# Optimization experiments

Hardware: AMD Instinct MI355X
Metric: run time of the kernel (lower is better)

## Reference

```python
import jax, jax.numpy as jnp
import numpy as np

DIM = 128        # channel dim C
N = 784          # H*W = 28*28 = max_seq_len
PBD = 128        # position_bias_dim
FF = 4 * DIM
EPS_LN = 1e-5


def layer_norm(x, g, b):
    mu = jnp.mean(x, axis=-1, keepdims=True)
    var = jnp.mean((x - mu) ** 2, axis=-1, keepdims=True)
    return (x - mu) * jax.lax.rsqrt(var + EPS_LN) * g + b


def setup_inputs() -> dict:
    key = jax.random.key(0)
    ks = jax.random.split(key, 12)
    s = 0.02
    return {
        "x": jax.random.normal(ks[0], (1, DIM, 28, 28), dtype=jnp.float32),
        "wq": jax.random.normal(ks[1], (DIM, DIM), dtype=jnp.float32) * s,
        "wk": jax.random.normal(ks[2], (DIM, DIM), dtype=jnp.float32) * s,
        "wv": jax.random.normal(ks[3], (DIM, DIM), dtype=jnp.float32) * s,
        "wo": jax.random.normal(ks[4], (DIM, DIM), dtype=jnp.float32) * s,
        "bo": jnp.zeros((DIM,), dtype=jnp.float32),
        "u": jax.random.normal(ks[5], (N, PBD), dtype=jnp.float32) * 0.01,
        "v": jax.random.normal(ks[6], (N, PBD), dtype=jnp.float32) * 0.01,
        "ln1_g": jnp.ones((DIM,), dtype=jnp.float32),
        "ln1_b": jnp.zeros((DIM,), dtype=jnp.float32),
        "ln2_g": jnp.ones((DIM,), dtype=jnp.float32),
        "ln2_b": jnp.zeros((DIM,), dtype=jnp.float32),
        "w1": jax.random.normal(ks[7], (FF, DIM), dtype=jnp.float32) * s,
        "b1": jnp.zeros((FF,), dtype=jnp.float32),
        "w2": jax.random.normal(ks[8], (DIM, FF), dtype=jnp.float32) * s,
        "b2": jnp.zeros((DIM,), dtype=jnp.float32),
    }


def reference(x, wq, wk, wv, wo, bo, u, v, ln1_g, ln1_b, ln2_g, ln2_b, w1, b1, w2, b2):
    B, C, H, W = x.shape
    t = x.reshape(B, C, H * W).transpose(0, 2, 1)  # [B, N, C]

    # --- AFT-Full attention block ---
    xn = layer_norm(t, ln1_g, ln1_b)
    q = jax.nn.sigmoid(xn @ wq.T)                  # [B, N, D]
    k = xn @ wk.T                                  # [B, N, D]
    vv = xn @ wv.T                                 # [B, N, D]
    pos_bias = u @ v.T                             # [N, N] (query n, key m)
    logits = k[:, None, :, :] + pos_bias[None, :, :, None]  # [B, N, M, D]
    attn = jax.nn.softmax(logits, axis=2)          # softmax over key axis m
    ctx = jnp.einsum('bnmd,bmd->bnd', attn, vv)    # weighted sum over keys
    out = q * ctx                                  # sigmoid gate (dropout=identity)
    out = out @ wo.T + bo
    t = t + out

    # --- MLP block ---
    fn = layer_norm(t, ln2_g, ln2_b)
    ff = jax.nn.gelu(fn @ w1.T + b1, approximate=False) @ w2.T + b2
    t = t + ff

    return t.transpose(0, 2, 1).reshape(B, C, H, W)
```

## Files before the change

kernel.cpp:

```cpp
#include <hip/hip_runtime.h>
#include <math.h>

#define NTOK 784
#define DIM 128
#define FFD 512

__global__ __launch_bounds__(256) void posw_qkv3(
    const float* __restrict__ pu, const float* __restrict__ pv, float* __restrict__ W,
    const float* __restrict__ x, const float* __restrict__ g, const float* __restrict__ b,
    const float* __restrict__ wq, const float* __restrict__ wk, const float* __restrict__ wv,
    float* __restrict__ q, float* __restrict__ ek, float* __restrict__ vv) {
  __shared__ float smem[12288];
  int tid = threadIdx.x;

  if (blockIdx.x < 325) {
    float (*As)[32] = (float(*)[32])smem;
    float (*Bs)[64] = (float(*)[64])(smem + 4096);
    int m0 = (blockIdx.x % 25) * 32, n0 = (blockIdx.x / 25) * 64;
    {
      int r = tid >> 3, kq = (tid & 7) * 16;
      int gm = min(m0 + r, NTOK - 1);
#pragma unroll
      for (int j = 0; j < 4; ++j) {
        float4 a = *(const float4*)&pu[gm * DIM + kq + j * 4];
        As[kq + j * 4 + 0][r] = a.x; As[kq + j * 4 + 1][r] = a.y;
        As[kq + j * 4 + 2][r] = a.z; As[kq + j * 4 + 3][r] = a.w;
      }
      int rb = tid >> 2, kb = (tid & 3) * 32;
      int gn = min(n0 + rb, NTOK - 1);
#pragma unroll
      for (int j = 0; j < 8; ++j) {
        float4 v = *(const float4*)&pv[gn * DIM + kb + j * 4];
        Bs[kb + j * 4 + 0][rb] = v.x; Bs[kb + j * 4 + 1][rb] = v.y;
        Bs[kb + j * 4 + 2][rb] = v.z; Bs[kb + j * 4 + 3][rb] = v.w;
      }
    }
    __syncthreads();
    int tx = tid & 15, ty = tid >> 4;
    float acc[2][4] = {};
#pragma unroll 8
    for (int kk = 0; kk < DIM; ++kk) {
      float2 a2 = *(const float2*)&As[kk][ty * 2];
      float4 b4 = *(const float4*)&Bs[kk][tx * 4];
      float av[2] = {a2.x, a2.y};
      float bv[4] = {b4.x, b4.y, b4.z, b4.w};
#pragma unroll
      for (int i = 0; i < 2; ++i)
#pragma unroll
        for (int j = 0; j < 4; ++j) acc[i][j] = fmaf(av[i], bv[j], acc[i][j]);
    }
    int c0 = n0 + tx * 4;
    if (c0 + 3 < NTOK) {
#pragma unroll
      for (int i = 0; i < 2; ++i) {
        int gr = m0 + ty * 2 + i;
        if (gr < NTOK) {
          float4 o = {expf(acc[i][0]), expf(acc[i][1]), expf(acc[i][2]), expf(acc[i][3])};
          *(float4*)&W[gr * NTOK + c0] = o;
        }
      }
    }
  } else {
    float (*Xs)[32] = (float(*)[32])smem;
    float (*Bq)[64] = (float(*)[64])(smem + 4096);
    float* redS = smem + 8192;
    float* redQ = smem + 8448;
    int bid = blockIdx.x - 325;
    int m0 = (bid % 25) * 32;
    int ct = bid / 25;
    int wsel = ct >> 1;
    int n0 = (ct & 1) * 64;
    const float* B = (wsel == 0) ? wq : (wsel == 1) ? wk : wv;

    if (m0 + 32 <= NTOK) {
#pragma unroll
      for (int it = 0; it < 4; ++it) {
        int idx = it * 256 + tid;
        int c = idx >> 3, j4 = (idx & 7) * 4;
        float4 v = *(const float4*)&x[c * NTOK + m0 + j4];
        Xs[c][j4 + 0] = v.x; Xs[c][j4 + 1] = v.y; Xs[c][j4 + 2] = v.z; Xs[c][j4 + 3] = v.w;
      }
    } else {
#pragma unroll
      for (int it = 0; it < 4; ++it) {
        int idx = it * 256 + tid;
        int c = idx >> 3, j4 = (idx & 7) * 4;
#pragma unroll
        for (int u = 0; u < 4; ++u) {
          int n = min(m0 + j4 + u, NTOK - 1);
          Xs[c][j4 + u] = x[c * NTOK + n];
        }
      }
    }
    __syncthreads();

    int n = tid & 31, grp = tid >> 5;
    float s = 0.f, ss = 0.f;
    for (int c = grp * 16; c < grp * 16 + 16; ++c) { float v = Xs[c][n]; s += v; ss += v * v; }
    redS[grp * 32 + n] = s; redQ[grp * 32 + n] = ss;
    __syncthreads();
    float sum = 0.f, sq = 0.f;
#pragma unroll
    for (int gi = 0; gi < 8; ++gi) { sum += redS[gi * 32 + n]; sq += redQ[gi * 32 + n]; }
    float mu = sum * (1.0f / DIM);
    float var = sq * (1.0f / DIM) - mu * mu;
    float rs = rsqrtf(var + 1e-5f);
    for (int c = grp * 16; c < grp * 16 + 16; ++c)
      Xs[c][n] = (Xs[c][n] - mu) * rs * g[c] + b[c];

    int tx = tid & 15, ty = tid >> 4;
    float acc[2][4] = {};
#pragma unroll
    for (int h = 0; h < 2; ++h) {
      {
        int r = tid >> 2, kq = (tid & 3) * 16;
#pragma unroll
        for (int j = 0; j < 4; ++j) {
          float4 v = *(const float4*)&B[(n0 + r) * DIM + h * 64 + kq + j * 4];
          Bq[kq + j * 4 + 0][r] = v.x; Bq[kq + j * 4 + 1][r] = v.y;
          Bq[kq + j * 4 + 2][r] = v.z; Bq[kq + j * 4 + 3][r] = v.w;
        }
      }
      __syncthreads();
#pragma unroll 4
      for (int kk = 0; kk < 64; ++kk) {
        float2 a2 = *(const float2*)&Xs[h * 64 + kk][ty * 2];
        float4 b4 = *(const float4*)&Bq[kk][tx * 4];
        float av[2] = {a2.x, a2.y};
        float bv[4] = {b4.x, b4.y, b4.z, b4.w};
#pragma unroll
        for (int i = 0; i < 2; ++i)
#pragma unroll
          for (int j = 0; j < 4; ++j) acc[i][j] = fmaf(av[i], bv[j], acc[i][j]);
      }
      __syncthreads();
    }
    int c0 = n0 + tx * 4;
    float* dst = (wsel == 0) ? q : (wsel == 1) ? ek : vv;
#pragma unroll
    for (int i = 0; i < 2; ++i) {
      int gr = m0 + ty * 2 + i;
      if (gr < NTOK) {
        float4 o;
        if (wsel == 0) {
          o.x = 1.0f / (1.0f + expf(-acc[i][0]));
          o.y = 1.0f / (1.0f + expf(-acc[i][1]));
          o.z = 1.0f / (1.0f + expf(-acc[i][2]));
          o.w = 1.0f / (1.0f + expf(-acc[i][3]));
        } else if (wsel == 1) {
          o.x = expf(acc[i][0]); o.y = expf(acc[i][1]);
          o.z = expf(acc[i][2]); o.w = expf(acc[i][3]);
        } else {
          o.x = acc[i][0]; o.y = acc[i][1]; o.z = acc[i][2]; o.w = acc[i][3];
        }
        *(float4*)&dst[gr * DIM + c0] = o;
      }
    }
  }
}

__global__ __launch_bounds__(256) void agg32(
    const float* __restrict__ W, const float* __restrict__ ek,
    const float* __restrict__ vv, float* __restrict__ nump, float* __restrict__ denp) {
  __shared__ float As[96][32];
  __shared__ float Bn[96][64];
  __shared__ float Bd[96][64];
  int tid = threadIdx.x;
  int m0 = blockIdx.x * 32, d0 = blockIdx.y * 64, sp = blockIdx.z;
  int tx = tid & 15, ty = tid >> 4;
  int ra = tid >> 3, ka = (tid & 7) * 4;
  int kb = tid >> 3, db = (tid & 7) * 8;
  int gm = min(m0 + ra, NTOK - 1);
  float an[2][4] = {}, ad[2][4] = {};
  int tlo = (sp * 25) / 8, thi = ((sp + 1) * 25) / 8;
  for (int base = tlo; base < thi; base += 3) {
    int nt = min(3, thi - base);
    for (int t = 0; t < nt; ++t) {
      int k0 = (base + t) * 32;
      int lk = t * 32;
      if (k0 + 32 <= NTOK) {
        float4 a = *(const float4*)&W[gm * NTOK + k0 + ka];
        As[lk + ka + 0][ra] = a.x; As[lk + ka + 1][ra] = a.y;
        As[lk + ka + 2][ra] = a.z; As[lk + ka + 3][ra] = a.w;
        int gk = k0 + kb;
        float4 e0 = *(const float4*)&ek[gk * DIM + d0 + db];
        float4 e1 = *(const float4*)&ek[gk * DIM + d0 + db + 4];
        float4 w0 = *(const float4*)&vv[gk * DIM + d0 + db];
        float4 w1_ = *(const float4*)&vv[gk * DIM + d0 + db + 4];
        Bd[lk + kb][db + 0] = e0.x; Bd[lk + kb][db + 1] = e0.y;
        Bd[lk + kb][db + 2] = e0.z; Bd[lk + kb][db + 3] = e0.w;
        Bd[lk + kb][db + 4] = e1.x; Bd[lk + kb][db + 5] = e1.y;
        Bd[lk + kb][db + 6] = e1.z; Bd[lk + kb][db + 7] = e1.w;
        Bn[lk + kb][db + 0] = e0.x * w0.x; Bn[lk + kb][db + 1] = e0.y * w0.y;
        Bn[lk + kb][db + 2] = e0.z * w0.z; Bn[lk + kb][db + 3] = e0.w * w0.w;
        Bn[lk + kb][db + 4] = e1.x * w1_.x; Bn[lk + kb][db + 5] = e1.y * w1_.y;
        Bn[lk + kb][db + 6] = e1.z * w1_.z; Bn[lk + kb][db + 7] = e1.w * w1_.w;
      } else {
#pragma unroll
        for (int j = 0; j < 4; ++j) {
          int gk = k0 + ka + j;
          As[lk + ka + j][ra] = (gk < NTOK) ? W[gm * NTOK + gk] : 0.f;
        }
        int gk = k0 + kb;
        if (gk < NTOK) {
          float4 e0 = *(const float4*)&ek[gk * DIM + d0 + db];
          float4 e1 = *(const float4*)&ek[gk * DIM + d0 + db + 4];
          float4 w0 = *(const float4*)&vv[gk * DIM + d0 + db];
          float4 w1_ = *(const float4*)&vv[gk * DIM + d0 + db + 4];
          Bd[lk + kb][db + 0] = e0.x; Bd[lk + kb][db + 1] = e0.y;
          Bd[lk + kb][db + 2] = e0.z; Bd[lk + kb][db + 3] = e0.w;
          Bd[lk + kb][db + 4] = e1.x; Bd[lk + kb][db + 5] = e1.y;
          Bd[lk + kb][db + 6] = e1.z; Bd[lk + kb][db + 7] = e1.w;
          Bn[lk + kb][db + 0] = e0.x * w0.x; Bn[lk + kb][db + 1] = e0.y * w0.y;
          Bn[lk + kb][db + 2] = e0.z * w0.z; Bn[lk + kb][db + 3] = e0.w * w0.w;
          Bn[lk + kb][db + 4] = e1.x * w1_.x; Bn[lk + kb][db + 5] = e1.y * w1_.y;
          Bn[lk + kb][db + 6] = e1.z * w1_.z; Bn[lk + kb][db + 7] = e1.w * w1_.w;
        } else {
#pragma unroll
          for (int j = 0; j < 8; ++j) { Bd[lk + kb][db + j] = 0.f; Bn[lk + kb][db + j] = 0.f; }
        }
      }
    }
    __syncthreads();
    int nk = nt * 32;
    for (int kk = 0; kk < nk; ++kk) {
      float2 a2 = *(const float2*)&As[kk][ty * 2];
      float4 n4 = *(const float4*)&Bn[kk][tx * 4];
      float4 d4 = *(const float4*)&Bd[kk][tx * 4];
      float av[2] = {a2.x, a2.y};
      float nv[4] = {n4.x, n4.y, n4.z, n4.w};
      float dv[4] = {d4.x, d4.y, d4.z, d4.w};
#pragma unroll
      for (int i = 0; i < 2; ++i)
#pragma unroll
        for (int j = 0; j < 4; ++j) {
          an[i][j] = fmaf(av[i], nv[j], an[i][j]);
          ad[i][j] = fmaf(av[i], dv[j], ad[i][j]);
        }
    }
    __syncthreads();
  }
#pragma unroll
  for (int i = 0; i < 2; ++i) {
    int gr = m0 + ty * 2 + i;
    if (gr < NTOK) {
      float4 on = {an[i][0], an[i][1], an[i][2], an[i][3]};
      float4 od = {ad[i][0], ad[i][1], ad[i][2], ad[i][3]};
      *(float4*)&nump[(sp * NTOK + gr) * DIM + d0 + tx * 4] = on;
      *(float4*)&denp[(sp * NTOK + gr) * DIM + d0 + tx * 4] = od;
    }
  }
}

__global__ __launch_bounds__(256) void gate_proj_ln(
    const float* __restrict__ q, const float* __restrict__ nump,
    const float* __restrict__ denp, const float* __restrict__ wo,
    const float* __restrict__ bo, const float* __restrict__ x,
    const float* __restrict__ g2, const float* __restrict__ b2n,
    const float* __restrict__ b2f, float* __restrict__ fn, float* __restrict__ out) {
  __shared__ float At[DIM][9];
  __shared__ float Bs[DIM][DIM];
  int tid = threadIdx.x;
  int m0 = blockIdx.x * 8;

  {
    int nn = tid >> 5, c4 = (tid & 31) * 4;
    int base = (m0 + nn) * DIM + c4;
    float4 qv = *(const float4*)&q[base];
    float4 nv = {0.f, 0.f, 0.f, 0.f}, dv = {0.f, 0.f, 0.f, 0.f};
#pragma unroll
    for (int s = 0; s < 8; ++s) {
      float4 a = *(const float4*)&nump[s * NTOK * DIM + base];
      float4 d = *(const float4*)&denp[s * NTOK * DIM + base];
      nv.x += a.x; nv.y += a.y; nv.z += a.z; nv.w += a.w;
      dv.x += d.x; dv.y += d.y; dv.z += d.z; dv.w += d.w;
    }
    At[c4 + 0][nn] = qv.x * (nv.x / dv.x);
    At[c4 + 1][nn] = qv.y * (nv.y / dv.y);
    At[c4 + 2][nn] = qv.z * (nv.z / dv.z);
    At[c4 + 3][nn] = qv.w * (nv.w / dv.w);
  }
  {
    int r = tid >> 1, kq = (tid & 1) * 64;
#pragma unroll
    for (int j = 0; j < 16; ++j) {
      float4 v = *(const float4*)&wo[r * DIM + kq + j * 4];
      Bs[kq + j * 4 + 0][r] = v.x; Bs[kq + j * 4 + 1][r] = v.y;
      Bs[kq + j * 4 + 2][r] = v.z; Bs[kq + j * 4 + 3][r] = v.w;
    }
  }
  __syncthreads();

  int ty = tid >> 5, tx = tid & 31;
  float acc[4] = {0.f, 0.f, 0.f, 0.f};
#pragma unroll 4
  for (int kk = 0; kk < DIM; ++kk) {
    float a = At[kk][ty];
    float4 b4 = *(const float4*)&Bs[kk][tx * 4];
    acc[0] = fmaf(a, b4.x, acc[0]);
    acc[1] = fmaf(a, b4.y, acc[1]);
    acc[2] = fmaf(a, b4.z, acc[2]);
    acc[3] = fmaf(a, b4.w, acc[3]);
  }
  int gn = m0 + ty;
  int c0 = tx * 4;
  float4 bias = *(const float4*)&bo[c0];
  float o0 = acc[0] + bias.x + x[(c0 + 0) * NTOK + gn];
  float o1 = acc[1] + bias.y + x[(c0 + 1) * NTOK + gn];
  float o2 = acc[2] + bias.z + x[(c0 + 2) * NTOK + gn];
  float o3 = acc[3] + bias.w + x[(c0 + 3) * NTOK + gn];

  float4 bf = *(const float4*)&b2f[c0];
  out[(c0 + 0) * NTOK + gn] = o0 + bf.x;
  out[(c0 + 1) * NTOK + gn] = o1 + bf.y;
  out[(c0 + 2) * NTOK + gn] = o2 + bf.z;
  out[(c0 + 3) * NTOK + gn] = o3 + bf.w;

  float s = o0 + o1 + o2 + o3;
  float ss = o0 * o0 + o1 * o1 + o2 * o2 + o3 * o3;
#pragma unroll
  for (int off = 1; off < 32; off <<= 1) {
    s += __shfl_xor(s, off);
    ss += __shfl_xor(ss, off);
  }
  float mu = s * (1.0f / DIM);
  float var = ss * (1.0f / DIM) - mu * mu;
  float rs = rsqrtf(var + 1e-5f);
  float4 gg = *(const float4*)&g2[c0];
  float4 bb = *(const float4*)&b2n[c0];
  float4 f;
  f.x = (o0 - mu) * rs * gg.x + bb.x;
  f.y = (o1 - mu) * rs * gg.y + bb.y;
  f.z = (o2 - mu) * rs * gg.z + bb.z;
  f.w = (o3 - mu) * rs * gg.w + bb.w;
  *(float4*)&fn[gn * DIM + c0] = f;
}

__global__ __launch_bounds__(256) void ff_fused16(
    const float* __restrict__ fn, const float* __restrict__ w1,
    const float* __restrict__ b1f, const float* __restrict__ w2,
    float* __restrict__ out) {
  __shared__ float Fs[DIM][16];
  __shared__ float W1s[DIM][64];
  __shared__ float P[16][65];
  int tid = threadIdx.x;
  int m0 = blockIdx.x * 16, f0 = blockIdx.y * 64;

  {
    int r = tid >> 4, kq = (tid & 15) * 8;
#pragma unroll
    for (int j = 0; j < 2; ++j) {
      float4 v = *(const float4*)&fn[(m0 + r) * DIM + kq + j * 4];
      Fs[kq + j * 4 + 0][r] = v.x; Fs[kq + j * 4 + 1][r] = v.y;
      Fs[kq + j * 4 + 2][r] = v.z; Fs[kq + j * 4 + 3][r] = v.w;
    }
    int rw = tid >> 2, kw = (tid & 3) * 32;
#pragma unroll
    for (int j = 0; j < 8; ++j) {
      float4 v = *(const float4*)&w1[(f0 + rw) * DIM + kw + j * 4];
      W1s[kw + j * 4 + 0][rw] = v.x; W1s[kw + j * 4 + 1][rw] = v.y;
      W1s[kw + j * 4 + 2][rw] = v.z; W1s[kw + j * 4 + 3][rw] = v.w;
    }
  }
  __syncthreads();

  int row = tid >> 4, f4 = (tid & 15) * 4;
  float acc1[4] = {};
#pragma unroll 4
  for (int kk = 0; kk < DIM; ++kk) {
    float a = Fs[kk][row];
    float4 b4 = *(const float4*)&W1s[kk][f4];
    acc1[0] = fmaf(a, b4.x, acc1[0]);
    acc1[1] = fmaf(a, b4.y, acc1[1]);
    acc1[2] = fmaf(a, b4.z, acc1[2]);
    acc1[3] = fmaf(a, b4.w, acc1[3]);
  }
  float4 b1v = *(const float4*)&b1f[f0 + f4];
  float bb[4] = {b1v.x, b1v.y, b1v.z, b1v.w};
  float ge[4];
#pragma unroll
  for (int j = 0; j < 4; ++j) {
    float v = acc1[j] + bb[j];
    ge[j] = 0.5f * v * (1.0f + erff(v * 0.70710678118654752f));
  }
  __syncthreads();

#pragma unroll
  for (int j = 0; j < 4; ++j) P[row][f4 + j] = ge[j];
  float* W2s = &W1s[0][0];
  {
    int c = tid >> 1, fq = (tid & 1) * 32;
#pragma unroll
    for (int j = 0; j < 8; ++j) {
      float4 v = *(const float4*)&w2[c * FFD + f0 + fq + j * 4];
      W2s[(fq + j * 4 + 0) * DIM + c] = v.x;
      W2s[(fq + j * 4 + 1) * DIM + c] = v.y;
      W2s[(fq + j * 4 + 2) * DIM + c] = v.z;
      W2s[(fq + j * 4 + 3) * DIM + c] = v.w;
    }
  }
  __syncthreads();

  int r2 = tid & 15, cb = (tid >> 4) * 8;
  float acc2[8] = {};
  for (int f = 0; f < 64; ++f) {
    float pvv = P[r2][f];
    const float* wr = &W2s[f * DIM + cb];
#pragma unroll
    for (int j4 = 0; j4 < 2; ++j4) {
      float4 wv = *(const float4*)&wr[j4 * 4];
      acc2[j4 * 4 + 0] = fmaf(pvv, wv.x, acc2[j4 * 4 + 0]);
      acc2[j4 * 4 + 1] = fmaf(pvv, wv.y, acc2[j4 * 4 + 1]);
      acc2[j4 * 4 + 2] = fmaf(pvv, wv.z, acc2[j4 * 4 + 2]);
      acc2[j4 * 4 + 3] = fmaf(pvv, wv.w, acc2[j4 * 4 + 3]);
    }
  }
#pragma unroll
  for (int j = 0; j < 8; ++j)
    atomicAdd(&out[(cb + j) * NTOK + m0 + r2], acc2[j]);
}

extern "C" void kernel_launch(void* const* d_in, const int* in_sizes, int n_in,
                              void* d_out, int out_size, void* d_ws, size_t ws_size,
                              hipStream_t stream) {
  const float* x   = (const float*)d_in[0];
  const float* wq  = (const float*)d_in[1];
  const float* wk  = (const float*)d_in[2];
  const float* wv  = (const float*)d_in[3];
  const float* wo  = (const float*)d_in[4];
  const float* bo  = (const float*)d_in[5];
  const float* pu  = (const float*)d_in[6];
  const float* pv  = (const float*)d_in[7];
  const float* g1  = (const float*)d_in[8];
  const float* b1n = (const float*)d_in[9];
  const float* g2  = (const float*)d_in[10];
  const float* b2n = (const float*)d_in[11];
  const float* w1  = (const float*)d_in[12];
  const float* b1f = (const float*)d_in[13];
  const float* w2  = (const float*)d_in[14];
  const float* b2f = (const float*)d_in[15];
  float* out = (float*)d_out;

  float* ws = (float*)d_ws;
  float* q    = ws;
  float* ek   = ws + 100352;
  float* vv   = ws + 200704;
  float* fn   = ws + 301056;
  float* W    = ws + 401408;
  float* nump = ws + 1016064;
  float* denp = ws + 1818880;

  posw_qkv3<<<475, 256, 0, stream>>>(pu, pv, W, x, g1, b1n, wq, wk, wv, q, ek, vv);
  agg32<<<dim3(25, 2, 8), 256, 0, stream>>>(W, ek, vv, nump, denp);
  gate_proj_ln<<<98, 256, 0, stream>>>(q, nump, denp, wo, bo, x, g2, b2n, b2f, fn, out);
  ff_fused16<<<dim3(49, 8), 256, 0, stream>>>(fn, w1, b1f, w2, out);
}
```

Before: 50.35 us.

## Fuse gate/out-projection/LN2 with the MLP into one kernel and zero output early

Merges the gate+output projection+LayerNorm kernel with the fused MLP kernel, so each of the 8 FF-slice blocks per 8-token tile recomputes the attention gate, the Wo projection and LN2 in shared memory instead of writing and re-reading the normalized activations. The output buffer is zeroed inside the first kernel, and the residual is folded into the blockIdx.y==0 atomic contribution. This removes one kernel launch and the fn round trip through global memory. In exchange the Wo projection and the nump/denp reduction are repeated eight times, shared memory grows to about 70KB, and the FF tiles shrink to 8 tokens, which may lower occupancy.

```diff
diff --git a/kernel.cpp b/kernel.cpp
--- a/kernel.cpp
+++ b/kernel.cpp
@@ -9,9 +9,12 @@
     const float* __restrict__ pu, const float* __restrict__ pv, float* __restrict__ W,
     const float* __restrict__ x, const float* __restrict__ g, const float* __restrict__ b,
     const float* __restrict__ wq, const float* __restrict__ wk, const float* __restrict__ wv,
-    float* __restrict__ q, float* __restrict__ ek, float* __restrict__ vv) {
+    float* __restrict__ q, float* __restrict__ ek, float* __restrict__ vv,
+    float* __restrict__ out) {
   __shared__ float smem[12288];
   int tid = threadIdx.x;
+
+  for (int i = blockIdx.x * 256 + tid; i < NTOK * DIM; i += 475 * 256) out[i] = 0.f;
 
   if (blockIdx.x < 325) {
     float (*As)[32] = (float(*)[32])smem;
@@ -252,16 +255,21 @@
   }
 }
 
-__global__ __launch_bounds__(256) void gate_proj_ln(
+__global__ __launch_bounds__(256) void epi_fused(
     const float* __restrict__ q, const float* __restrict__ nump,
     const float* __restrict__ denp, const float* __restrict__ wo,
     const float* __restrict__ bo, const float* __restrict__ x,
     const float* __restrict__ g2, const float* __restrict__ b2n,
-    const float* __restrict__ b2f, float* __restrict__ fn, float* __restrict__ out) {
+    const float* __restrict__ w1, const float* __restrict__ b1f,
+    const float* __restrict__ w2, const float* __restrict__ b2f,
+    float* __restrict__ out) {
   __shared__ float At[DIM][9];
-  __shared__ float Bs[DIM][DIM];
+  __shared__ float Ws[DIM * DIM];
+  __shared__ float Fn[DIM][9];
+  __shared__ float P[64][9];
   int tid = threadIdx.x;
   int m0 = blockIdx.x * 8;
+  int f0 = blockIdx.y * 64;
 
   {
     int nn = tid >> 5, c4 = (tid & 31) * 4;
@@ -285,139 +293,109 @@
 #pragma unroll
     for (int j = 0; j < 16; ++j) {
       float4 v = *(const float4*)&wo[r * DIM + kq + j * 4];
-      Bs[kq + j * 4 + 0][r] = v.x; Bs[kq + j * 4 + 1][r] = v.y;
-      Bs[kq + j * 4 + 2][r] = v.z; Bs[kq + j * 4 + 3][r] = v.w;
+      Ws[(kq + j * 4 + 0) * DIM + r] = v.x; Ws[(kq + j * 4 + 1) * DIM + r] = v.y;
+      Ws[(kq + j * 4 + 2) * DIM + r] = v.z; Ws[(kq + j * 4 + 3) * DIM + r] = v.w;
     }
   }
   __syncthreads();
 
-  int ty = tid >> 5, tx = tid & 31;
-  float acc[4] = {0.f, 0.f, 0.f, 0.f};
+  int row = tid >> 5, c4 = (tid & 31) * 4;
+  int gn = m0 + row;
+  float tv[4];
+  {
+    float acc[4] = {0.f, 0.f, 0.f, 0.f};
 #pragma unroll 4
-  for (int kk = 0; kk < DIM; ++kk) {
-    float a = At[kk][ty];
-    float4 b4 = *(const float4*)&Bs[kk][tx * 4];
-    acc[0] = fmaf(a, b4.x, acc[0]);
-    acc[1] = fmaf(a, b4.y, acc[1]);
-    acc[2] = fmaf(a, b4.z, acc[2]);
-    acc[3] = fmaf(a, b4.w, acc[3]);
-  }
-  int gn = m0 + ty;
-  int c0 = tx * 4;
-  float4 bias = *(const float4*)&bo[c0];
-  float o0 = acc[0] + bias.x + x[(c0 + 0) * NTOK + gn];
-  float o1 = acc[1] + bias.y + x[(c0 + 1) * NTOK + gn];
-  float o2 = acc[2] + bias.z + x[(c0 + 2) * NTOK + gn];
-  float o3 = acc[3] + bias.w + x[(c0 + 3) * NTOK + gn];
-
-  float4 bf = *(const float4*)&b2f[c0];
-  out[(c0 + 0) * NTOK + gn] = o0 + bf.x;
-  out[(c0 + 1) * NTOK + gn] = o1 + bf.y;
-  out[(c0 + 2) * NTOK + gn] = o2 + bf.z;
-  out[(c0 + 3) * NTOK + gn] = o3 + bf.w;
-
-  float s = o0 + o1 + o2 + o3;
-  float ss = o0 * o0 + o1 * o1 + o2 * o2 + o3 * o3;
-#pragma unroll
-  for (int off = 1; off < 32; off <<= 1) {
-    s += __shfl_xor(s, off);
-    ss += __shfl_xor(ss, off);
-  }
-  float mu = s * (1.0f / DIM);
-  float var = ss * (1.0f / DIM) - mu * mu;
-  float rs = rsqrtf(var + 1e-5f);
-  float4 gg = *(const float4*)&g2[c0];
-  float4 bb = *(const float4*)&b2n[c0];
-  float4 f;
-  f.x = (o0 - mu) * rs * gg.x + bb.x;
-  f.y = (o1 - mu) * rs * gg.y + bb.y;
-  f.z = (o2 - mu) * rs * gg.z + bb.z;
-  f.w = (o3 - mu) * rs * gg.w + bb.w;
-  *(float4*)&fn[gn * DIM + c0] = f;
-}
-
-__global__ __launch_bounds__(256) void ff_fused16(
-    const float* __restrict__ fn, const float* __restrict__ w1,
-    const float* __restrict__ b1f, const float* __restrict__ w2,
-    float* __restrict__ out) {
-  __shared__ float Fs[DIM][16];
-  __shared__ float W1s[DIM][64];
-  __shared__ float P[16][65];
-  int tid = threadIdx.x;
-  int m0 = blockIdx.x * 16, f0 = blockIdx.y * 64;
-
-  {
-    int r = tid >> 4, kq = (tid & 15) * 8;
-#pragma unroll
-    for (int j = 0; j < 2; ++j) {
-      float4 v = *(const float4*)&fn[(m0 + r) * DIM + kq + j * 4];
-      Fs[kq + j * 4 + 0][r] = v.x; Fs[kq + j * 4 + 1][r] = v.y;
-      Fs[kq + j * 4 + 2][r] = v.z; Fs[kq + j * 4 + 3][r] = v.w;
-    }
+    for (int kk = 0; kk < DIM; ++kk) {
+      float a = At[kk][row];
+      float4 b4 = *(const float4*)&Ws[kk * DIM + c4];
+      acc[0] = fmaf(a, b4.x, acc[0]);
+      acc[1] = fmaf(a, b4.y, acc[1]);
+      acc[2] = fmaf(a, b4.z, acc[2]);
+      acc[3] = fmaf(a, b4.w, acc[3]);
+    }
+    float4 bias = *(const float4*)&bo[c4];
+    float o0 = acc[0] + bias.x + x[(c4 + 0) * NTOK + gn];
+    float o1 = acc[1] + bias.y + x[(c4 + 1) * NTOK + gn];
+    float o2 = acc[2] + bias.z + x[(c4 + 2) * NTOK + gn];
+    float o3 = acc[3] + bias.w + x[(c4 + 3) * NTOK + gn];
+    float4 bf = *(const float4*)&b2f[c4];
+    tv[0] = o0 + bf.x; tv[1] = o1 + bf.y; tv[2] = o2 + bf.z; tv[3] = o3 + bf.w;
+
+    float s = o0 + o1 + o2 + o3;
+    float ss = o0 * o0 + o1 * o1 + o2 * o2 + o3 * o3;
+#pragma unroll
+    for (int off = 1; off < 32; off <<= 1) {
+      s += __shfl_xor(s, off);
+      ss += __shfl_xor(ss, off);
+    }
+    float mu = s * (1.0f / DIM);
+    float var = ss * (1.0f / DIM) - mu * mu;
+    float rs = rsqrtf(var + 1e-5f);
+    float4 gg = *(const float4*)&g2[c4];
+    float4 bb = *(const float4*)&b2n[c4];
+    Fn[c4 + 0][row] = (o0 - mu) * rs * gg.x + bb.x;
+    Fn[c4 + 1][row] = (o1 - mu) * rs * gg.y + bb.y;
+    Fn[c4 + 2][row] = (o2 - mu) * rs * gg.z + bb.z;
+    Fn[c4 + 3][row] = (o3 - mu) * rs * gg.w + bb.w;
+  }
+  __syncthreads();
+
+  {
     int rw = tid >> 2, kw = (tid & 3) * 32;
 #pragma unroll
     for (int j = 0; j < 8; ++j) {
       float4 v = *(const float4*)&w1[(f0 + rw) * DIM + kw + j * 4];
-      W1s[kw + j * 4 + 0][rw] = v.x; W1s[kw + j * 4 + 1][rw] = v.y;
-      W1s[kw + j * 4 + 2][rw] = v.z; W1s[kw + j * 4 + 3][rw] = v.w;
-    }
-  }
-  __syncthreads();
-
-  int row = tid >> 4, f4 = (tid & 15) * 4;
-  float acc1[4] = {};
-#pragma unroll 4
-  for (int kk = 0; kk < DIM; ++kk) {
-    float a = Fs[kk][row];
-    float4 b4 = *(const float4*)&W1s[kk][f4];
-    acc1[0] = fmaf(a, b4.x, acc1[0]);
-    acc1[1] = fmaf(a, b4.y, acc1[1]);
-    acc1[2] = fmaf(a, b4.z, acc1[2]);
-    acc1[3] = fmaf(a, b4.w, acc1[3]);
-  }
-  float4 b1v = *(const float4*)&b1f[f0 + f4];
-  float bb[4] = {b1v.x, b1v.y, b1v.z, b1v.w};
-  float ge[4];
-#pragma unroll
-  for (int j = 0; j < 4; ++j) {
-    float v = acc1[j] + bb[j];
-    ge[j] = 0.5f * v * (1.0f + erff(v * 0.70710678118654752f));
-  }
-  __syncthreads();
-
-#pragma unroll
-  for (int j = 0; j < 4; ++j) P[row][f4 + j] = ge[j];
-  float* W2s = &W1s[0][0];
-  {
+      Ws[(kw + j * 4 + 0) * 64 + rw] = v.x; Ws[(kw + j * 4 + 1) * 64 + rw] = v.y;
+      Ws[(kw + j * 4 + 2) * 64 + rw] = v.z; Ws[(kw + j * 4 + 3) * 64 + rw] = v.w;
+    }
+    float* W2s = Ws + 8192;
     int c = tid >> 1, fq = (tid & 1) * 32;
 #pragma unroll
     for (int j = 0; j < 8; ++j) {
       float4 v = *(const float4*)&w2[c * FFD + f0 + fq + j * 4];
-      W2s[(fq + j * 4 + 0) * DIM + c] = v.x;
-      W2s[(fq + j * 4 + 1) * DIM + c] = v.y;
-      W2s[(fq + j * 4 + 2) * DIM + c] = v.z;
-      W2s[(fq + j * 4 + 3) * DIM + c] = v.w;
+      W2s[(fq + j * 4 + 0) * DIM + c] = v.x; W2s[(fq + j * 4 + 1) * DIM + c] = v.y;
+      W2s[(fq + j * 4 + 2) * DIM + c] = v.z; W2s[(fq + j * 4 + 3) * DIM + c] = v.w;
     }
   }
   __syncthreads();
 
-  int r2 = tid & 15, cb = (tid >> 4) * 8;
-  float acc2[8] = {};
-  for (int f = 0; f < 64; ++f) {
-    float pvv = P[r2][f];
-    const float* wr = &W2s[f * DIM + cb];
-#pragma unroll
-    for (int j4 = 0; j4 < 2; ++j4) {
-      float4 wv = *(const float4*)&wr[j4 * 4];
-      acc2[j4 * 4 + 0] = fmaf(pvv, wv.x, acc2[j4 * 4 + 0]);
-      acc2[j4 * 4 + 1] = fmaf(pvv, wv.y, acc2[j4 * 4 + 1]);
-      acc2[j4 * 4 + 2] = fmaf(pvv, wv.z, acc2[j4 * 4 + 2]);
-      acc2[j4 * 4 + 3] = fmaf(pvv, wv.w, acc2[j4 * 4 + 3]);
-    }
-  }
-#pragma unroll
-  for (int j = 0; j < 8; ++j)
-    atomicAdd(&out[(cb + j) * NTOK + m0 + r2], acc2[j]);
+  {
+    int f2 = (tid & 31) * 2;
+    float a0 = 0.f, a1 = 0.f;
+#pragma unroll 4
+    for (int kk = 0; kk < DIM; ++kk) {
+      float a = Fn[kk][row];
+      float2 w = *(const float2*)&Ws[kk * 64 + f2];
+      a0 = fmaf(a, w.x, a0);
+      a1 = fmaf(a, w.y, a1);
+    }
+    float2 b1v = *(const float2*)&b1f[f0 + f2];
+    float v0 = a0 + b1v.x, v1 = a1 + b1v.y;
+    P[f2 + 0][row] = 0.5f * v0 * (1.0f + erff(v0 * 0.70710678118654752f));
+    P[f2 + 1][row] = 0.5f * v1 * (1.0f + erff(v1 * 0.70710678118654752f));
+  }
+  __syncthreads();
+
+  {
+    const float* W2s = Ws + 8192;
+    float acc[4] = {0.f, 0.f, 0.f, 0.f};
+#pragma unroll 4
+    for (int f = 0; f < 64; ++f) {
+      float p = P[f][row];
+      float4 w4 = *(const float4*)&W2s[f * DIM + c4];
+      acc[0] = fmaf(p, w4.x, acc[0]);
+      acc[1] = fmaf(p, w4.y, acc[1]);
+      acc[2] = fmaf(p, w4.z, acc[2]);
+      acc[3] = fmaf(p, w4.w, acc[3]);
+    }
+    if (blockIdx.y == 0) {
+      acc[0] += tv[0]; acc[1] += tv[1]; acc[2] += tv[2]; acc[3] += tv[3];
+    }
+    atomicAdd(&out[(c4 + 0) * NTOK + gn], acc[0]);
+    atomicAdd(&out[(c4 + 1) * NTOK + gn], acc[1]);
+    atomicAdd(&out[(c4 + 2) * NTOK + gn], acc[2]);
+    atomicAdd(&out[(c4 + 3) * NTOK + gn], acc[3]);
+  }
 }
 
 extern "C" void kernel_launch(void* const* d_in, const int* in_sizes, int n_in,
@@ -445,13 +423,12 @@
   float* q    = ws;
   float* ek   = ws + 100352;
   float* vv   = ws + 200704;
-  float* fn   = ws + 301056;
-  float* W    = ws + 401408;
-  float* nump = ws + 1016064;
-  float* denp = ws + 1818880;
-
-  posw_qkv3<<<475, 256, 0, stream>>>(pu, pv, W, x, g1, b1n, wq, wk, wv, q, ek, vv);
+  float* W    = ws + 301056;
+  float* nump = ws + 915712;
+  float* denp = ws + 1718528;
+
+  posw_qkv3<<<475, 256, 0, stream>>>(pu, pv, W, x, g1, b1n, wq, wk, wv, q, ek, vv, out);
   agg32<<<dim3(25, 2, 8), 256, 0, stream>>>(W, ek, vv, nump, denp);
-  gate_proj_ln<<<98, 256, 0, stream>>>(q, nump, denp, wo, bo, x, g2, b2n, b2f, fn, out);
-  ff_fused16<<<dim3(49, 8), 256, 0, stream>>>(fn, w1, b1f, w2, out);
+  epi_fused<<<dim3(98, 8), 256, 0, stream>>>(q, nump, denp, wo, bo, x, g2, b2n,
+                                             w1, b1f, w2, b2f, out);
 }
```

Result: slower. 77.76 us (+54.4%).

## Replace split-K aggregation with full-K per-block reduction and fuse gating

Applied to the files above, without the earlier changes.

The aggregation kernel no longer splits the key dimension into 8 partial sums. Each block now holds 8 full rows of the positional-weight matrix in shared memory, iterates over all 784 keys with register prefetch of the next ek/vv tile, and applies the sigmoid gate and division in place, writing the final attention output. This removes the large partial-sum buffers and the reduction pass in the projection kernel. The cost is a smaller grid of 196 blocks with low per-thread arithmetic (2 columns each), about 33KB of shared memory per block, and a longer serial loop per block.

```diff
diff --git a/kernel.cpp b/kernel.cpp
--- a/kernel.cpp
+++ b/kernel.cpp
@@ -159,102 +159,97 @@
   }
 }
 
-__global__ __launch_bounds__(256) void agg32(
+__global__ __launch_bounds__(256) void agg_full(
     const float* __restrict__ W, const float* __restrict__ ek,
-    const float* __restrict__ vv, float* __restrict__ nump, float* __restrict__ denp) {
-  __shared__ float As[96][32];
-  __shared__ float Bn[96][64];
-  __shared__ float Bd[96][64];
+    const float* __restrict__ vv, const float* __restrict__ q,
+    float* __restrict__ attn) {
+  __shared__ float Wt[8 * 784];
+  __shared__ float Bd[32][68];
+  __shared__ float Bn[32][68];
   int tid = threadIdx.x;
-  int m0 = blockIdx.x * 32, d0 = blockIdx.y * 64, sp = blockIdx.z;
-  int tx = tid & 15, ty = tid >> 4;
-  int ra = tid >> 3, ka = (tid & 7) * 4;
-  int kb = tid >> 3, db = (tid & 7) * 8;
-  int gm = min(m0 + ra, NTOK - 1);
-  float an[2][4] = {}, ad[2][4] = {};
-  int tlo = (sp * 25) / 8, thi = ((sp + 1) * 25) / 8;
-  for (int base = tlo; base < thi; base += 3) {
-    int nt = min(3, thi - base);
-    for (int t = 0; t < nt; ++t) {
-      int k0 = (base + t) * 32;
-      int lk = t * 32;
-      if (k0 + 32 <= NTOK) {
-        float4 a = *(const float4*)&W[gm * NTOK + k0 + ka];
-        As[lk + ka + 0][ra] = a.x; As[lk + ka + 1][ra] = a.y;
-        As[lk + ka + 2][ra] = a.z; As[lk + ka + 3][ra] = a.w;
-        int gk = k0 + kb;
-        float4 e0 = *(const float4*)&ek[gk * DIM + d0 + db];
-        float4 e1 = *(const float4*)&ek[gk * DIM + d0 + db + 4];
-        float4 w0 = *(const float4*)&vv[gk * DIM + d0 + db];
-        float4 w1_ = *(const float4*)&vv[gk * DIM + d0 + db + 4];
-        Bd[lk + kb][db + 0] = e0.x; Bd[lk + kb][db + 1] = e0.y;
-        Bd[lk + kb][db + 2] = e0.z; Bd[lk + kb][db + 3] = e0.w;
-        Bd[lk + kb][db + 4] = e1.x; Bd[lk + kb][db + 5] = e1.y;
-        Bd[lk + kb][db + 6] = e1.z; Bd[lk + kb][db + 7] = e1.w;
-        Bn[lk + kb][db + 0] = e0.x * w0.x; Bn[lk + kb][db + 1] = e0.y * w0.y;
-        Bn[lk + kb][db + 2] = e0.z * w0.z; Bn[lk + kb][db + 3] = e0.w * w0.w;
-        Bn[lk + kb][db + 4] = e1.x * w1_.x; Bn[lk + kb][db + 5] = e1.y * w1_.y;
-        Bn[lk + kb][db + 6] = e1.z * w1_.z; Bn[lk + kb][db + 7] = e1.w * w1_.w;
-      } else {
-#pragma unroll
-        for (int j = 0; j < 4; ++j) {
-          int gk = k0 + ka + j;
-          As[lk + ka + j][ra] = (gk < NTOK) ? W[gm * NTOK + gk] : 0.f;
-        }
-        int gk = k0 + kb;
-        if (gk < NTOK) {
-          float4 e0 = *(const float4*)&ek[gk * DIM + d0 + db];
-          float4 e1 = *(const float4*)&ek[gk * DIM + d0 + db + 4];
-          float4 w0 = *(const float4*)&vv[gk * DIM + d0 + db];
-          float4 w1_ = *(const float4*)&vv[gk * DIM + d0 + db + 4];
-          Bd[lk + kb][db + 0] = e0.x; Bd[lk + kb][db + 1] = e0.y;
-          Bd[lk + kb][db + 2] = e0.z; Bd[lk + kb][db + 3] = e0.w;
-          Bd[lk + kb][db + 4] = e1.x; Bd[lk + kb][db + 5] = e1.y;
-          Bd[lk + kb][db + 6] = e1.z; Bd[lk + kb][db + 7] = e1.w;
-          Bn[lk + kb][db + 0] = e0.x * w0.x; Bn[lk + kb][db + 1] = e0.y * w0.y;
-          Bn[lk + kb][db + 2] = e0.z * w0.z; Bn[lk + kb][db + 3] = e0.w * w0.w;
-          Bn[lk + kb][db + 4] = e1.x * w1_.x; Bn[lk + kb][db + 5] = e1.y * w1_.y;
-          Bn[lk + kb][db + 6] = e1.z * w1_.z; Bn[lk + kb][db + 7] = e1.w * w1_.w;
-        } else {
-#pragma unroll
-          for (int j = 0; j < 8; ++j) { Bd[lk + kb][db + j] = 0.f; Bn[lk + kb][db + j] = 0.f; }
-        }
-      }
+  int m0 = blockIdx.x * 8, d0 = blockIdx.y * 64;
+
+#pragma unroll
+  for (int j = 0; j < 7; ++j) {
+    int idx = j * 256 + tid;
+    if (idx < 1568) {
+      int r = idx / 196, c4 = (idx % 196) * 4;
+      float4 a = *(const float4*)&W[(m0 + r) * NTOK + c4];
+      *(float4*)&Wt[r * 784 + c4] = a;
+    }
+  }
+
+  int ks = tid >> 4, d4 = (tid & 15) * 4;
+  float4 pe0, pe1, pv0, pv1;
+  {
+    pe0 = *(const float4*)&ek[(ks)*DIM + d0 + d4];
+    pv0 = *(const float4*)&vv[(ks)*DIM + d0 + d4];
+    pe1 = *(const float4*)&ek[(16 + ks) * DIM + d0 + d4];
+    pv1 = *(const float4*)&vv[(16 + ks) * DIM + d0 + d4];
+  }
+
+  int row = tid >> 5, c2 = (tid & 31) * 2;
+  float an0 = 0.f, an1 = 0.f, ad0 = 0.f, ad1 = 0.f;
+  const float* wr = &Wt[row * 784];
+
+  for (int c = 0; c < 25; ++c) {
+    int k0 = c * 32;
+    int nk = (k0 + 32 <= NTOK) ? 32 : (NTOK - k0);
+    if (ks < nk) {
+      Bd[ks][d4 + 0] = pe0.x; Bd[ks][d4 + 1] = pe0.y; Bd[ks][d4 + 2] = pe0.z; Bd[ks][d4 + 3] = pe0.w;
+      Bn[ks][d4 + 0] = pe0.x * pv0.x; Bn[ks][d4 + 1] = pe0.y * pv0.y;
+      Bn[ks][d4 + 2] = pe0.z * pv0.z; Bn[ks][d4 + 3] = pe0.w * pv0.w;
+    }
+    if (16 + ks < nk) {
+      Bd[16 + ks][d4 + 0] = pe1.x; Bd[16 + ks][d4 + 1] = pe1.y;
+      Bd[16 + ks][d4 + 2] = pe1.z; Bd[16 + ks][d4 + 3] = pe1.w;
+      Bn[16 + ks][d4 + 0] = pe1.x * pv1.x; Bn[16 + ks][d4 + 1] = pe1.y * pv1.y;
+      Bn[16 + ks][d4 + 2] = pe1.z * pv1.z; Bn[16 + ks][d4 + 3] = pe1.w * pv1.w;
     }
     __syncthreads();
-    int nk = nt * 32;
-    for (int kk = 0; kk < nk; ++kk) {
-      float2 a2 = *(const float2*)&As[kk][ty * 2];
-      float4 n4 = *(const float4*)&Bn[kk][tx * 4];
-      float4 d4 = *(const float4*)&Bd[kk][tx * 4];
-      float av[2] = {a2.x, a2.y};
-      float nv[4] = {n4.x, n4.y, n4.z, n4.w};
-      float dv[4] = {d4.x, d4.y, d4.z, d4.w};
-#pragma unroll
-      for (int i = 0; i < 2; ++i)
-#pragma unroll
-        for (int j = 0; j < 4; ++j) {
-          an[i][j] = fmaf(av[i], nv[j], an[i][j]);
-          ad[i][j] = fmaf(av[i], dv[j], ad[i][j]);
-        }
+    if (c < 24) {
+      int kn = (c + 1) * 32;
+      int nkn = (kn + 32 <= NTOK) ? 32 : (NTOK - kn);
+      if (ks < nkn) {
+        pe0 = *(const float4*)&ek[(kn + ks) * DIM + d0 + d4];
+        pv0 = *(const float4*)&vv[(kn + ks) * DIM + d0 + d4];
+      }
+      if (16 + ks < nkn) {
+        pe1 = *(const float4*)&ek[(kn + 16 + ks) * DIM + d0 + d4];
+        pv1 = *(const float4*)&vv[(kn + 16 + ks) * DIM + d0 + d4];
+      }
+    }
+    if (nk == 32) {
+#pragma unroll 8
+      for (int kk = 0; kk < 32; ++kk) {
+        float a = wr[k0 + kk];
+        float2 bn = *(const float2*)&Bn[kk][c2];
+        float2 bd = *(const float2*)&Bd[kk][c2];
+        an0 = fmaf(a, bn.x, an0); an1 = fmaf(a, bn.y, an1);
+        ad0 = fmaf(a, bd.x, ad0); ad1 = fmaf(a, bd.y, ad1);
+      }
+    } else {
+#pragma unroll 8
+      for (int kk = 0; kk < 16; ++kk) {
+        float a = wr[k0 + kk];
+        float2 bn = *(const float2*)&Bn[kk][c2];
+        float2 bd = *(const float2*)&Bd[kk][c2];
+        an0 = fmaf(a, bn.x, an0); an1 = fmaf(a, bn.y, an1);
+        ad0 = fmaf(a, bd.x, ad0); ad1 = fmaf(a, bd.y, ad1);
+      }
     }
     __syncthreads();
   }
-#pragma unroll
-  for (int i = 0; i < 2; ++i) {
-    int gr = m0 + ty * 2 + i;
-    if (gr < NTOK) {
-      float4 on = {an[i][0], an[i][1], an[i][2], an[i][3]};
-      float4 od = {ad[i][0], ad[i][1], ad[i][2], ad[i][3]};
-      *(float4*)&nump[(sp * NTOK + gr) * DIM + d0 + tx * 4] = on;
-      *(float4*)&denp[(sp * NTOK + gr) * DIM + d0 + tx * 4] = od;
-    }
-  }
+
+  int gn = m0 + row;
+  int cc = d0 + c2;
+  float2 qv = *(const float2*)&q[gn * DIM + cc];
+  float2 o = {qv.x * (an0 / ad0), qv.y * (an1 / ad1)};
+  *(float2*)&attn[gn * DIM + cc] = o;
 }
 
-__global__ __launch_bounds__(256) void gate_proj_ln(
-    const float* __restrict__ q, const float* __restrict__ nump,
-    const float* __restrict__ denp, const float* __restrict__ wo,
+__global__ __launch_bounds__(256) void proj_ln(
+    const float* __restrict__ attn, const float* __restrict__ wo,
     const float* __restrict__ bo, const float* __restrict__ x,
     const float* __restrict__ g2, const float* __restrict__ b2n,
     const float* __restrict__ b2f, float* __restrict__ fn, float* __restrict__ out) {
@@ -265,20 +260,9 @@
 
   {
     int nn = tid >> 5, c4 = (tid & 31) * 4;
-    int base = (m0 + nn) * DIM + c4;
-    float4 qv = *(const float4*)&q[base];
-    float4 nv = {0.f, 0.f, 0.f, 0.f}, dv = {0.f, 0.f, 0.f, 0.f};
-#pragma unroll
-    for (int s = 0; s < 8; ++s) {
-      float4 a = *(const float4*)&nump[s * NTOK * DIM + base];
-      float4 d = *(const float4*)&denp[s * NTOK * DIM + base];
-      nv.x += a.x; nv.y += a.y; nv.z += a.z; nv.w += a.w;
-      dv.x += d.x; dv.y += d.y; dv.z += d.z; dv.w += d.w;
-    }
-    At[c4 + 0][nn] = qv.x * (nv.x / dv.x);
-    At[c4 + 1][nn] = qv.y * (nv.y / dv.y);
-    At[c4 + 2][nn] = qv.z * (nv.z / dv.z);
-    At[c4 + 3][nn] = qv.w * (nv.w / dv.w);
+    float4 av = *(const float4*)&attn[(m0 + nn) * DIM + c4];
+    At[c4 + 0][nn] = av.x; At[c4 + 1][nn] = av.y;
+    At[c4 + 2][nn] = av.z; At[c4 + 3][nn] = av.w;
   }
   {
     int r = tid >> 1, kq = (tid & 1) * 64;
@@ -446,12 +430,11 @@
   float* ek   = ws + 100352;
   float* vv   = ws + 200704;
   float* fn   = ws + 301056;
-  float* W    = ws + 401408;
-  float* nump = ws + 1016064;
-  float* denp = ws + 1818880;
+  float* attn = ws + 401408;
+  float* W    = ws + 501760;
 
   posw_qkv3<<<475, 256, 0, stream>>>(pu, pv, W, x, g1, b1n, wq, wk, wv, q, ek, vv);
-  agg32<<<dim3(25, 2, 8), 256, 0, stream>>>(W, ek, vv, nump, denp);
-  gate_proj_ln<<<98, 256, 0, stream>>>(q, nump, denp, wo, bo, x, g2, b2n, b2f, fn, out);
+  agg_full<<<dim3(98, 2), 256, 0, stream>>>(W, ek, vv, q, attn);
+  proj_ln<<<98, 256, 0, stream>>>(attn, wo, bo, x, g2, b2n, b2f, fn, out);
   ff_fused16<<<dim3(49, 8), 256, 0, stream>>>(fn, w1, b1f, w2, out);
 }
```

New measurement: 67.86 us. 34.8% more time.

## Fold gate/projection/LayerNorm into aggregation kernel via last-block-done atomic counter

Applied to the files above, without the earlier changes.

The separate gate_proj_ln launch is removed. Each row tile of the aggregation kernel increments an atomic counter after writing its partial numerators and denominators. The 16th block to finish for that tile (2 d-halves × 8 splits) reduces the partials, applies the sigmoid gate, multiplies by wo, adds the residual and computes LayerNorm2. This saves one kernel launch and its tail, but the final work runs on only 25 elected blocks instead of 98, and it adds threadfence and atomic overhead. The counters are zeroed in the first kernel.

```diff
diff --git a/kernel.cpp b/kernel.cpp
--- a/kernel.cpp
+++ b/kernel.cpp
@@ -9,9 +9,12 @@
     const float* __restrict__ pu, const float* __restrict__ pv, float* __restrict__ W,
     const float* __restrict__ x, const float* __restrict__ g, const float* __restrict__ b,
     const float* __restrict__ wq, const float* __restrict__ wk, const float* __restrict__ wv,
-    float* __restrict__ q, float* __restrict__ ek, float* __restrict__ vv) {
+    float* __restrict__ q, float* __restrict__ ek, float* __restrict__ vv,
+    int* __restrict__ cnt) {
   __shared__ float smem[12288];
   int tid = threadIdx.x;
+
+  if (blockIdx.x == 0 && tid < 32) cnt[tid] = 0;
 
   if (blockIdx.x < 325) {
     float (*As)[32] = (float(*)[32])smem;
@@ -159,12 +162,18 @@
   }
 }
 
-__global__ __launch_bounds__(256) void agg32(
+__global__ __launch_bounds__(256) void agg32_fold(
     const float* __restrict__ W, const float* __restrict__ ek,
-    const float* __restrict__ vv, float* __restrict__ nump, float* __restrict__ denp) {
-  __shared__ float As[96][32];
-  __shared__ float Bn[96][64];
-  __shared__ float Bd[96][64];
+    const float* __restrict__ vv, float* __restrict__ nump, float* __restrict__ denp,
+    const float* __restrict__ q, const float* __restrict__ wo,
+    const float* __restrict__ bo, const float* __restrict__ x,
+    const float* __restrict__ g2, const float* __restrict__ b2n,
+    const float* __restrict__ b2f, float* __restrict__ fn, float* __restrict__ out,
+    int* __restrict__ cnt) {
+  __shared__ float smem[15360];
+  float (*As)[32] = (float(*)[32])smem;
+  float (*Bn)[64] = (float(*)[64])(smem + 3072);
+  float (*Bd)[64] = (float(*)[64])(smem + 9216);
   int tid = threadIdx.x;
   int m0 = blockIdx.x * 32, d0 = blockIdx.y * 64, sp = blockIdx.z;
   int tx = tid & 15, ty = tid >> 4;
@@ -250,90 +259,115 @@
       *(float4*)&denp[(sp * NTOK + gr) * DIM + d0 + tx * 4] = od;
     }
   }
-}
-
-__global__ __launch_bounds__(256) void gate_proj_ln(
-    const float* __restrict__ q, const float* __restrict__ nump,
-    const float* __restrict__ denp, const float* __restrict__ wo,
-    const float* __restrict__ bo, const float* __restrict__ x,
-    const float* __restrict__ g2, const float* __restrict__ b2n,
-    const float* __restrict__ b2f, float* __restrict__ fn, float* __restrict__ out) {
-  __shared__ float At[DIM][9];
-  __shared__ float Bs[DIM][DIM];
-  int tid = threadIdx.x;
-  int m0 = blockIdx.x * 8;
+
+  __shared__ int elect;
+  __threadfence();
+  if (tid == 0) {
+    int old = atomicAdd(&cnt[blockIdx.x], 1);
+    elect = (old == 15) ? 1 : 0;
+  }
+  __syncthreads();
+  if (!elect) return;
+  __threadfence();
+
+  float (*Att)[33] = (float(*)[33])smem;
+  float (*Bs)[64] = (float(*)[64])(smem + 4224);
+  int row = tid >> 3, lane = tid & 7;
+  int gn = m0 + row;
+  bool live = (gn < NTOK);
+  int gc = min(gn, NTOK - 1);
 
   {
-    int nn = tid >> 5, c4 = (tid & 31) * 4;
-    int base = (m0 + nn) * DIM + c4;
-    float4 qv = *(const float4*)&q[base];
-    float4 nv = {0.f, 0.f, 0.f, 0.f}, dv = {0.f, 0.f, 0.f, 0.f};
-#pragma unroll
-    for (int s = 0; s < 8; ++s) {
-      float4 a = *(const float4*)&nump[s * NTOK * DIM + base];
-      float4 d = *(const float4*)&denp[s * NTOK * DIM + base];
-      nv.x += a.x; nv.y += a.y; nv.z += a.z; nv.w += a.w;
-      dv.x += d.x; dv.y += d.y; dv.z += d.z; dv.w += d.w;
-    }
-    At[c4 + 0][nn] = qv.x * (nv.x / dv.x);
-    At[c4 + 1][nn] = qv.y * (nv.y / dv.y);
-    At[c4 + 2][nn] = qv.z * (nv.z / dv.z);
-    At[c4 + 3][nn] = qv.w * (nv.w / dv.w);
-  }
-  {
-    int r = tid >> 1, kq = (tid & 1) * 64;
-#pragma unroll
-    for (int j = 0; j < 16; ++j) {
-      float4 v = *(const float4*)&wo[r * DIM + kq + j * 4];
-      Bs[kq + j * 4 + 0][r] = v.x; Bs[kq + j * 4 + 1][r] = v.y;
-      Bs[kq + j * 4 + 2][r] = v.z; Bs[kq + j * 4 + 3][r] = v.w;
+    int c16 = lane * 16;
+#pragma unroll
+    for (int j4 = 0; j4 < 4; ++j4) {
+      int c = c16 + j4 * 4;
+      int basei = gc * DIM + c;
+      float4 qv = *(const float4*)&q[basei];
+      float4 nv = {0.f, 0.f, 0.f, 0.f}, dv = {0.f, 0.f, 0.f, 0.f};
+#pragma unroll
+      for (int s = 0; s < 8; ++s) {
+        float4 a = *(const float4*)&nump[s * NTOK * DIM + basei];
+        float4 d = *(const float4*)&denp[s * NTOK * DIM + basei];
+        nv.x += a.x; nv.y += a.y; nv.z += a.z; nv.w += a.w;
+        dv.x += d.x; dv.y += d.y; dv.z += d.z; dv.w += d.w;
+      }
+      Att[c + 0][row] = qv.x * (nv.x / dv.x);
+      Att[c + 1][row] = qv.y * (nv.y / dv.y);
+      Att[c + 2][row] = qv.z * (nv.z / dv.z);
+      Att[c + 3][row] = qv.w * (nv.w / dv.w);
     }
   }
   __syncthreads();
 
-  int ty = tid >> 5, tx = tid & 31;
-  float acc[4] = {0.f, 0.f, 0.f, 0.f};
+  float o[16];
+  for (int ch = 0; ch < 2; ++ch) {
+    {
+      int r = tid >> 2, kq = (tid & 3) * 32;
+#pragma unroll
+      for (int j = 0; j < 8; ++j) {
+        float4 v = *(const float4*)&wo[(ch * 64 + r) * DIM + kq + j * 4];
+        Bs[kq + j * 4 + 0][r] = v.x; Bs[kq + j * 4 + 1][r] = v.y;
+        Bs[kq + j * 4 + 2][r] = v.z; Bs[kq + j * 4 + 3][r] = v.w;
+      }
+    }
+    __syncthreads();
+    int cl = lane * 8;
+    float acc[8] = {};
 #pragma unroll 4
-  for (int kk = 0; kk < DIM; ++kk) {
-    float a = At[kk][ty];
-    float4 b4 = *(const float4*)&Bs[kk][tx * 4];
-    acc[0] = fmaf(a, b4.x, acc[0]);
-    acc[1] = fmaf(a, b4.y, acc[1]);
-    acc[2] = fmaf(a, b4.z, acc[2]);
-    acc[3] = fmaf(a, b4.w, acc[3]);
-  }
-  int gn = m0 + ty;
-  int c0 = tx * 4;
-  float4 bias = *(const float4*)&bo[c0];
-  float o0 = acc[0] + bias.x + x[(c0 + 0) * NTOK + gn];
-  float o1 = acc[1] + bias.y + x[(c0 + 1) * NTOK + gn];
-  float o2 = acc[2] + bias.z + x[(c0 + 2) * NTOK + gn];
-  float o3 = acc[3] + bias.w + x[(c0 + 3) * NTOK + gn];
-
-  float4 bf = *(const float4*)&b2f[c0];
-  out[(c0 + 0) * NTOK + gn] = o0 + bf.x;
-  out[(c0 + 1) * NTOK + gn] = o1 + bf.y;
-  out[(c0 + 2) * NTOK + gn] = o2 + bf.z;
-  out[(c0 + 3) * NTOK + gn] = o3 + bf.w;
-
-  float s = o0 + o1 + o2 + o3;
-  float ss = o0 * o0 + o1 * o1 + o2 * o2 + o3 * o3;
-#pragma unroll
-  for (int off = 1; off < 32; off <<= 1) {
+    for (int k = 0; k < DIM; ++k) {
+      float a = Att[k][row];
+      float4 b0 = *(const float4*)&Bs[k][cl];
+      float4 b1 = *(const float4*)&Bs[k][cl + 4];
+      acc[0] = fmaf(a, b0.x, acc[0]); acc[1] = fmaf(a, b0.y, acc[1]);
+      acc[2] = fmaf(a, b0.z, acc[2]); acc[3] = fmaf(a, b0.w, acc[3]);
+      acc[4] = fmaf(a, b1.x, acc[4]); acc[5] = fmaf(a, b1.y, acc[5]);
+      acc[6] = fmaf(a, b1.z, acc[6]); acc[7] = fmaf(a, b1.w, acc[7]);
+    }
+#pragma unroll
+    for (int j = 0; j < 8; ++j) o[ch * 8 + j] = acc[j];
+    __syncthreads();
+  }
+
+  float s = 0.f, ss = 0.f;
+#pragma unroll
+  for (int i = 0; i < 16; ++i) {
+    int c = (i >> 3) * 64 + lane * 8 + (i & 7);
+    float val = o[i] + bo[c] + x[c * NTOK + gc];
+    o[i] = val; s += val; ss += val * val;
+  }
+#pragma unroll
+  for (int off = 1; off < 8; off <<= 1) {
     s += __shfl_xor(s, off);
     ss += __shfl_xor(ss, off);
   }
   float mu = s * (1.0f / DIM);
   float var = ss * (1.0f / DIM) - mu * mu;
   float rs = rsqrtf(var + 1e-5f);
-  float4 gg = *(const float4*)&g2[c0];
-  float4 bb = *(const float4*)&b2n[c0];
-  float4 f;
-  f.x = (o0 - mu) * rs * gg.x + bb.x;
-  f.y = (o1 - mu) * rs * gg.y + bb.y;
-  f.z = (o2 - mu) * rs * gg.z + bb.z;
-  f.w = (o3 - mu) * rs * gg.w + bb.w;
-  *(float4*)&fn[gn * DIM + c0] = f;
+
+  if (live) {
+#pragma unroll
+    for (int ch = 0; ch < 2; ++ch) {
+      int c0 = ch * 64 + lane * 8;
+      float4 f0, f1;
+      float* fp0 = &f0.x;
+      float* fp1 = &f1.x;
+#pragma unroll
+      for (int j = 0; j < 4; ++j) {
+        int c = c0 + j;
+        fp0[j] = (o[ch * 8 + j] - mu) * rs * g2[c] + b2n[c];
+        int c2 = c0 + 4 + j;
+        fp1[j] = (o[ch * 8 + 4 + j] - mu) * rs * g2[c2] + b2n[c2];
+      }
+      *(float4*)&fn[gn * DIM + c0] = f0;
+      *(float4*)&fn[gn * DIM + c0 + 4] = f1;
+#pragma unroll
+      for (int j = 0; j < 8; ++j) {
+        int c = c0 + j;
+        out[c * NTOK + gn] = o[ch * 8 + j] + b2f[c];
+      }
+    }
+  }
 }
 
 __global__ __launch_bounds__(256) void ff_fused16(
@@ -449,9 +483,10 @@
   float* W    = ws + 401408;
   float* nump = ws + 1016064;
   float* denp = ws + 1818880;
-
-  posw_qkv3<<<475, 256, 0, stream>>>(pu, pv, W, x, g1, b1n, wq, wk, wv, q, ek, vv);
-  agg32<<<dim3(25, 2, 8), 256, 0, stream>>>(W, ek, vv, nump, denp);
-  gate_proj_ln<<<98, 256, 0, stream>>>(q, nump, denp, wo, bo, x, g2, b2n, b2f, fn, out);
+  int*   cnt  = (int*)(ws + 2621696);
+
+  posw_qkv3<<<475, 256, 0, stream>>>(pu, pv, W, x, g1, b1n, wq, wk, wv, q, ek, vv, cnt);
+  agg32_fold<<<dim3(25, 2, 8), 256, 0, stream>>>(W, ek, vv, nump, denp, q, wo, bo, x,
+                                                 g2, b2n, b2f, fn, out, cnt);
   ff_fused16<<<dim3(49, 8), 256, 0, stream>>>(fn, w1, b1f, w2, out);
 }
```

New measurement: 102.0 us. 103% more time.
